# Optimization experiments

Measured on AMD Instinct MI355X. Metric: run time of the kernel, lower is better.

The kernel has to match this reference:

```python
import jax, jax.numpy as jnp
import numpy as np

B, T, D = 4, 4096, 2048
K = 1024
H, KVH, HD = 16, 4, 128
FF = 8192
EPS = 1e-6


def _rmsnorm(x, w):
    v = jnp.mean(x * x, axis=-1, keepdims=True)
    return x * jax.lax.rsqrt(v + EPS) * w


def _rotate_half(x):
    x1, x2 = jnp.split(x, 2, axis=-1)
    return jnp.concatenate([-x2, x1], axis=-1)


def setup_inputs() -> dict:
    key = jax.random.key(0)
    ks = jax.random.split(key, 16)
    hidden_states = jax.random.normal(ks[0], (B, T, D), dtype=jnp.float32)
    # unique sorted indices per sequence (top-k selection without duplicates)
    scores = jax.random.uniform(ks[1], (B, T))
    topk_indices = jnp.sort(jax.lax.top_k(scores, K)[1], axis=-1).astype(jnp.int64)
    gating_scores = jax.random.uniform(ks[2], (B, K), dtype=jnp.float32)
    # rotary embeddings over the full sequence [B, T, HD]
    inv = 1.0 / (10000.0 ** (jnp.arange(0, HD, 2, dtype=jnp.float32) / HD))
    ang = jnp.arange(T, dtype=jnp.float32)[:, None] * inv[None, :]  # [T, HD/2]
    emb = jnp.concatenate([ang, ang], axis=-1)
    cos = jnp.broadcast_to(jnp.cos(emb)[None], (B, T, HD)).astype(jnp.float32)
    sin = jnp.broadcast_to(jnp.sin(emb)[None], (B, T, HD)).astype(jnp.float32)
    s = 0.02
    params = dict(
        Wq=jax.random.normal(ks[3], (D, H * HD)) * s,
        bq=jnp.zeros((H * HD,)),
        Wk=jax.random.normal(ks[4], (D, KVH * HD)) * s,
        bk=jnp.zeros((KVH * HD,)),
        Wv=jax.random.normal(ks[5], (D, KVH * HD)) * s,
        bv=jnp.zeros((KVH * HD,)),
        Wo=jax.random.normal(ks[6], (H * HD, D)) * s,
        w_gate=jax.random.normal(ks[7], (D, FF)) * s,
        w_up=jax.random.normal(ks[8], (D, FF)) * s,
        w_down=jax.random.normal(ks[9], (FF, D)) * s,
        ln1_w=jnp.ones((D,)),
        ln2_w=jnp.ones((D,)),
    )
    return dict(hidden_states=hidden_states, topk_indices=topk_indices,
                gating_scores=gating_scores, cos=cos, sin=sin, **params)


def _decoder_layer(x, cos_s, sin_s, Wq, bq, Wk, bk, Wv, bv, Wo,
                   w_gate, w_up, w_down, ln1_w, ln2_w):
    # x: [B, K, D]; cos_s/sin_s: [B, K, HD]
    res = x
    h = _rmsnorm(x, ln1_w)
    q = (h @ Wq + bq).reshape(B, K, H, HD)
    k = (h @ Wk + bk).reshape(B, K, KVH, HD)
    v = (h @ Wv + bv).reshape(B, K, KVH, HD)
    c = cos_s[:, :, None, :]
    s = sin_s[:, :, None, :]
    q = q * c + _rotate_half(q) * s
    k = k * c + _rotate_half(k) * s
    # GQA: repeat kv heads
    k = jnp.repeat(k, H // KVH, axis=2)
    v = jnp.repeat(v, H // KVH, axis=2)
    scores = jnp.einsum('bqhd,bkhd->bhqk', q, k) / np.sqrt(HD)
    causal = jnp.tril(jnp.ones((K, K), dtype=bool))
    scores = jnp.where(causal[None, None], scores, jnp.finfo(scores.dtype).min)
    attn = jax.nn.softmax(scores, axis=-1)
    out = jnp.einsum('bhqk,bkhd->bqhd', attn, v).reshape(B, K, H * HD)
    x = res + out @ Wo
    # MLP (SwiGLU)
    res = x
    h = _rmsnorm(x, ln2_w)
    x = res + (jax.nn.silu(h @ w_gate) * (h @ w_up)) @ w_down
    return x


def reference(hidden_states, topk_indices, gating_scores, cos, sin,
              Wq, bq, Wk, bk, Wv, bv, Wo, w_gate, w_up, w_down, ln1_w, ln2_w):
    idx = topk_indices[:, :, None]  # [B, K, 1]
    selected = jnp.take_along_axis(hidden_states, idx, axis=1)  # [B, K, D]
    cos_s = jnp.take_along_axis(cos, idx, axis=1)
    sin_s = jnp.take_along_axis(sin, idx, axis=1)
    processed = _decoder_layer(selected, cos_s, sin_s, Wq, bq, Wk, bk, Wv, bv,
                               Wo, w_gate, w_up, w_down, ln1_w, ln2_w)
    # soft gating: selected + gate * (processed - selected)
    updated = selected + (processed - selected) * gating_scores[:, :, None]
    b_idx = jnp.arange(B)[:, None]
    final = hidden_states.at[b_idx, topk_indices].set(updated)
    return final
```

## Files before the change

kernel.cpp:

```cpp
#include <hip/hip_runtime.h>
#include <stdint.h>

typedef __bf16 bf16;
typedef __attribute__((ext_vector_type(8))) __bf16 bf16x8;
typedef __attribute__((ext_vector_type(4))) float f32x4;

namespace {

constexpr int cB = 4, cT = 4096, cD = 2048, cK = 1024, cH = 16, cKVH = 4, cHD = 128, cFF = 8192;
constexpr int cM = cB * cK;
constexpr int QKVW = cH * cHD + 2 * cKVH * cHD;

__device__ __forceinline__ void load_lds16(const void* g, void* l) {
  __builtin_amdgcn_global_load_lds((const __attribute__((address_space(1))) void*)g,
                                   (__attribute__((address_space(3))) void*)l, 16, 0, 0);
}

template <int N>
__device__ __forceinline__ void waitcnt_vm() {
  if constexpr (N == 0) asm volatile("s_waitcnt vmcnt(0)" ::: "memory");
  else if constexpr (N == 3) asm volatile("s_waitcnt vmcnt(3)" ::: "memory");
  else if constexpr (N == 4) asm volatile("s_waitcnt vmcnt(4)" ::: "memory");
  else if constexpr (N == 6) asm volatile("s_waitcnt vmcnt(6)" ::: "memory");
  else if constexpr (N == 8) asm volatile("s_waitcnt vmcnt(8)" ::: "memory");
  else if constexpr (N == 9) asm volatile("s_waitcnt vmcnt(9)" ::: "memory");
  else if constexpr (N == 12) asm volatile("s_waitcnt vmcnt(12)" ::: "memory");
  else static_assert(N == 0, "unsupported vmcnt literal");
}

template <int OP>
__device__ __forceinline__ float blk_reduce(float v) {
  __shared__ float sm[5];
  const int tid = threadIdx.x, lane = tid & 63, wid = tid >> 6;
#pragma unroll
  for (int o = 32; o; o >>= 1) {
    float o2 = __shfl_down(v, o, 64);
    v = OP ? fmaxf(v, o2) : v + o2;
  }
  if (lane == 0) sm[wid] = v;
  __syncthreads();
  if (tid == 0) {
    float r = sm[0];
#pragma unroll
    for (int i = 1; i < 4; ++i) r = OP ? fmaxf(r, sm[i]) : r + sm[i];
    sm[4] = r;
  }
  __syncthreads();
  float r = sm[4];
  __syncthreads();
  return r;
}

template <int BN, int WM, int WN, int RING, int UNROLL, class Epi>
__global__ __launch_bounds__(512, 2)
void gemm256(const bf16* __restrict__ A, int lda,
             const bf16* __restrict__ Bm, int ldb,
             int Kd, int GM, Epi epi) {
  constexpr int BM = 256;
  constexpr int FM = BM / WM / 16;
  constexpr int FN = BN / WN / 16;
  constexpr int ACALLS = 2;
  constexpr int BCALLS = BN / 128;
  constexpr int L = ACALLS + BCALLS;
  constexpr int D = RING - 1;
  constexpr int SLOTA = BM * 64;
  constexpr int SLOTB = BN * 64;
  constexpr int SLOT = SLOTA + SLOTB;
  __shared__ __align__(16) char lds[RING * SLOT];

  const int tid = threadIdx.x;
  const int lane = tid & 63;
  const int wid = tid >> 6;
  const int l15 = lane & 15, lq = lane >> 4;
  const int wr = wid / WN, wc = wid % WN;

  const int nwg = gridDim.x;
  const int xcd = blockIdx.x & 7, loc = blockIdx.x >> 3;
  const int wg = xcd * (nwg >> 3) + loc;
  const int GN = nwg / GM;
  const int per = 8 * GN;
  const int g = wg / per, r = wg % per;
  const int bm = g * 8 + (r & 7);
  const int bn = r >> 3;

  const bf16* Abase = A + (int64_t)bm * BM * lda;
  const bf16* Bbase = Bm + (int64_t)bn * BN * ldb;

  const bf16* srcA[ACALLS];
  int dstA[ACALLS];
#pragma unroll
  for (int c2 = 0; c2 < ACALLS; ++c2) {
    const int chunk = c2 * 512 + tid;
    const int row = chunk >> 2, pc = chunk & 3;
    const int lc = pc ^ ((row >> 1) & 3);
    srcA[c2] = Abase + (int64_t)row * lda + lc * 8;
    dstA[c2] = chunk * 16;
  }
  const bf16* srcB[BCALLS];
  int dstB[BCALLS];
#pragma unroll
  for (int c2 = 0; c2 < BCALLS; ++c2) {
    const int chunk = c2 * 512 + tid;
    const int row = chunk >> 2, pc = chunk & 3;
    const int lc = pc ^ ((row >> 1) & 3);
    srcB[c2] = Bbase + (int64_t)row * ldb + lc * 8;
    dstB[c2] = chunk * 16;
  }

  int offA[FM], offB[FN];
#pragma unroll
  for (int m = 0; m < FM; ++m) {
    const int row = wr * (BM / WM) + m * 16 + l15;
    offA[m] = row * 64 + (lq ^ ((row >> 1) & 3)) * 16;
  }
#pragma unroll
  for (int n = 0; n < FN; ++n) {
    const int row = wc * (BN / WN) + n * 16 + l15;
    offB[n] = SLOTA + row * 64 + (lq ^ ((row >> 1) & 3)) * 16;
  }

  const int KT = Kd >> 5;
  auto stage = [&](int t) {
    char* sb = lds + (size_t)(t % RING) * SLOT;
#pragma unroll
    for (int c2 = 0; c2 < ACALLS; ++c2)
      load_lds16(srcA[c2] + t * 32, sb + dstA[c2]);
#pragma unroll
    for (int c2 = 0; c2 < BCALLS; ++c2)
      load_lds16(srcB[c2] + t * 32, sb + SLOTA + dstB[c2]);
  };
  auto compute = [&](int t, f32x4 (&acc)[FM][FN]) {
    const char* sb = lds + (size_t)(t % RING) * SLOT;
    bf16x8 av[FM], bv[FN];
#pragma unroll
    for (int m = 0; m < FM; ++m) av[m] = *(const bf16x8*)(sb + offA[m]);
#pragma unroll
    for (int n = 0; n < FN; ++n) bv[n] = *(const bf16x8*)(sb + offB[n]);
    __builtin_amdgcn_s_setprio(1);
#pragma unroll
    for (int m = 0; m < FM; ++m)
#pragma unroll
      for (int n = 0; n < FN; ++n)
        acc[m][n] = __builtin_amdgcn_mfma_f32_16x16x32_bf16(av[m], bv[n], acc[m][n], 0, 0, 0);
    __builtin_amdgcn_s_setprio(0);
  };

  f32x4 acc[FM][FN] = {};

  if constexpr (UNROLL == 1) {
#pragma unroll
    for (int i = 0; i < D; ++i) stage(i);
    waitcnt_vm<(D - 1) * L>();
    __builtin_amdgcn_s_barrier();
    __builtin_amdgcn_sched_barrier(0);
    for (int t = 0; t < KT - D; ++t) {
      stage(t + D);
      compute(t, acc);
      waitcnt_vm<(D - 1) * L>();
      __builtin_amdgcn_s_barrier();
      __builtin_amdgcn_sched_barrier(0);
    }
    waitcnt_vm<0>();
    __builtin_amdgcn_s_barrier();
    for (int t = KT - D; t < KT; ++t) compute(t, acc);
  } else {
    static_assert(RING == 5 && UNROLL == 2, "pair mode is RING=5");
#pragma unroll
    for (int i = 0; i < 3; ++i) stage(i);
    waitcnt_vm<L>();
    __builtin_amdgcn_s_barrier();
    __builtin_amdgcn_sched_barrier(0);
    int t = 0;
    for (; t <= KT - 6; t += 2) {
      stage(t + 3);
      stage(t + 4);
      compute(t, acc);
      compute(t + 1, acc);
      waitcnt_vm<L>();
      __builtin_amdgcn_s_barrier();
      __builtin_amdgcn_sched_barrier(0);
    }
    stage(KT - 1);
    waitcnt_vm<0>();
    __builtin_amdgcn_s_barrier();
    compute(KT - 4, acc);
    compute(KT - 3, acc);
    compute(KT - 2, acc);
    compute(KT - 1, acc);
  }

#pragma unroll
  for (int m = 0; m < FM; ++m) {
    const int r0 = bm * BM + wr * (BM / WM) + m * 16 + lq * 4;
#pragma unroll
    for (int n = 0; n < FN; ++n) {
      const int c1 = bn * BN + wc * (BN / WN) + n * 16 + l15;
#pragma unroll
      for (int j = 0; j < 4; ++j) epi(r0 + j, c1, acc[m][n][j]);
    }
  }
}

__global__ __launch_bounds__(512, 2)
void gemm_gateup(const bf16* __restrict__ A, const bf16* __restrict__ Bg,
                 const bf16* __restrict__ Bu, bf16* __restrict__ act) {
  constexpr int BM = 256, BN = 128, WM = 4, WN = 2;
  constexpr int FM = 4, FN = 4;
  constexpr int RING = 4, D = 3, L = 4;
  constexpr int SLOTA = BM * 64, SLOTB = BN * 64;
  constexpr int SLOT = SLOTA + 2 * SLOTB;
  __shared__ __align__(16) char lds[RING * SLOT];

  const int tid = threadIdx.x;
  const int lane = tid & 63;
  const int wid = tid >> 6;
  const int l15 = lane & 15, lq = lane >> 4;
  const int wr = wid / WN, wc = wid % WN;

  const int nwg = gridDim.x;
  const int xcd = blockIdx.x & 7, loc = blockIdx.x >> 3;
  const int wg = xcd * (nwg >> 3) + loc;
  const int GM = 16, GN = nwg / GM;
  const int per = 8 * GN;
  const int g = wg / per, r = wg % per;
  const int bm = g * 8 + (r & 7);
  const int bn = r >> 3;

  const bf16* Abase = A + (int64_t)bm * BM * cD;
  const bf16* Gbase = Bg + (int64_t)bn * BN * cD;
  const bf16* Ubase = Bu + (int64_t)bn * BN * cD;

  const bf16* srcA[2];
  int dstA[2];
#pragma unroll
  for (int c2 = 0; c2 < 2; ++c2) {
    const int chunk = c2 * 512 + tid;
    const int row = chunk >> 2, pc = chunk & 3;
    const int lc = pc ^ ((row >> 1) & 3);
    srcA[c2] = Abase + (int64_t)row * cD + lc * 8;
    dstA[c2] = chunk * 16;
  }
  const int brow = tid >> 2, bpc = tid & 3;
  const int blc = bpc ^ ((brow >> 1) & 3);
  const bf16* srcG = Gbase + (int64_t)brow * cD + blc * 8;
  const bf16* srcU = Ubase + (int64_t)brow * cD + blc * 8;
  const int dstBo = tid * 16;

  int offA[FM], offB[FN];
#pragma unroll
  for (int m = 0; m < FM; ++m) {
    const int row = wr * 64 + m * 16 + l15;
    offA[m] = row * 64 + (lq ^ ((row >> 1) & 3)) * 16;
  }
#pragma unroll
  for (int n = 0; n < FN; ++n) {
    const int row = wc * 64 + n * 16 + l15;
    offB[n] = row * 64 + (lq ^ ((row >> 1) & 3)) * 16;
  }

  const int KT = cD >> 5;
  auto stage = [&](int t) {
    char* sb = lds + (size_t)(t % RING) * SLOT;
#pragma unroll
    for (int c2 = 0; c2 < 2; ++c2) load_lds16(srcA[c2] + t * 32, sb + dstA[c2]);
    load_lds16(srcG + t * 32, sb + SLOTA + dstBo);
    load_lds16(srcU + t * 32, sb + SLOTA + SLOTB + dstBo);
  };

  f32x4 accg[FM][FN] = {}, accu[FM][FN] = {};

  auto compute = [&](int t) {
    const char* sb = lds + (size_t)(t % RING) * SLOT;
    bf16x8 av[FM], gv[FN], uv[FN];
#pragma unroll
    for (int m = 0; m < FM; ++m) av[m] = *(const bf16x8*)(sb + offA[m]);
#pragma unroll
    for (int n = 0; n < FN; ++n) gv[n] = *(const bf16x8*)(sb + SLOTA + offB[n]);
#pragma unroll
    for (int n = 0; n < FN; ++n) uv[n] = *(const bf16x8*)(sb + SLOTA + SLOTB + offB[n]);
    __builtin_amdgcn_s_setprio(1);
#pragma unroll
    for (int m = 0; m < FM; ++m)
#pragma unroll
      for (int n = 0; n < FN; ++n) {
        accg[m][n] = __builtin_amdgcn_mfma_f32_16x16x32_bf16(av[m], gv[n], accg[m][n], 0, 0, 0);
        accu[m][n] = __builtin_amdgcn_mfma_f32_16x16x32_bf16(av[m], uv[n], accu[m][n], 0, 0, 0);
      }
    __builtin_amdgcn_s_setprio(0);
  };

#pragma unroll
  for (int i = 0; i < D; ++i) stage(i);
  waitcnt_vm<(D - 1) * L>();
  __builtin_amdgcn_s_barrier();
  __builtin_amdgcn_sched_barrier(0);
  for (int t = 0; t < KT - D; ++t) {
    stage(t + D);
    compute(t);
    waitcnt_vm<(D - 1) * L>();
    __builtin_amdgcn_s_barrier();
    __builtin_amdgcn_sched_barrier(0);
  }
  waitcnt_vm<0>();
  __builtin_amdgcn_s_barrier();
  for (int t = KT - D; t < KT; ++t) compute(t);

#pragma unroll
  for (int m = 0; m < FM; ++m) {
    const int r0 = bm * BM + wr * 64 + m * 16 + lq * 4;
#pragma unroll
    for (int n = 0; n < FN; ++n) {
      const int c1 = bn * BN + wc * 64 + n * 16 + l15;
#pragma unroll
      for (int j = 0; j < 4; ++j) {
        float gvv = accg[m][n][j];
        float s = gvv / (1.f + __expf(-gvv));
        act[(int64_t)(r0 + j) * cFF + c1] = (bf16)(s * accu[m][n][j]);
      }
    }
  }
}

struct EpiQKV {
  bf16* out; const float* bias;
  __device__ void operator()(int r, int c, float v) const {
    out[(int64_t)r * QKVW + c] = (bf16)(v + bias[c]);
  }
};
struct EpiOProj {
  float* x; const float* hidden; const int* topk;
  __device__ void operator()(int r, int c, float v) const {
    int b = r >> 10;
    int t = topk[r];
    x[(int64_t)r * cD + c] = v + hidden[((int64_t)b * cT + t) * cD + c];
  }
};
struct EpiDown {
  float* out; const float* x; const float* hidden; const int* topk; const float* gating;
  __device__ void operator()(int r, int c, float v) const {
    int b = r >> 10;
    int t = topk[r];
    float x2 = v + x[(int64_t)r * cD + c];
    int64_t ho = ((int64_t)b * cT + t) * cD + c;
    float sel = hidden[ho];
    out[ho] = sel + (x2 - sel) * gating[r];
  }
};

__global__ __launch_bounds__(256, 2) void flash_attn(const bf16* __restrict__ qkv,
                                                     const bf16* __restrict__ vt,
                                                     bf16* __restrict__ outb) {
  constexpr int QB = 64, KVB = 128;
  __shared__ __align__(16) char lds[81920];
  char* sK = lds;
  char* sP = lds + 32768;
  char* sV = lds + 49152;

  const int qt = blockIdx.x, h = blockIdx.y, b = blockIdx.z;
  const int kvh = h >> 2;
  const int qlo = qt * QB;
  const int tid = threadIdx.x, lane = tid & 63, wid = tid >> 6;
  const int l15 = lane & 15, lq = lane >> 4;
  const int wid16 = wid * 16;

  const bf16* qbase = qkv + (int64_t)(b * cK + qlo) * QKVW + h * cHD;
  const bf16* kbase = qkv + (int64_t)(b * cK) * QKVW + cH * cHD + kvh * cHD;
  const bf16* vtbase = vt + (int64_t)(b * cKVH + kvh) * cHD * cK;

#pragma unroll
  for (int c2 = 0; c2 < 4; ++c2) {
    int chunk = c2 * 256 + tid;
    int row = chunk >> 4, c16 = chunk & 15;
    load_lds16(qbase + (int64_t)row * QKVW + (c16 ^ (row & 15)) * 8, sK + chunk * 16);
  }
  __syncthreads();
  bf16x8 qf[4];
  {
    const int row = wid16 + l15;
#pragma unroll
    for (int kt = 0; kt < 4; ++kt)
      qf[kt] = *(const bf16x8*)(sK + row * 256 + (((kt * 4 + lq) ^ (row & 15)) * 16));
  }
  __syncthreads();

  f32x4 oacc[8] = {};
  float m_run[4], l_run[4];
#pragma unroll
  for (int j = 0; j < 4; ++j) { m_run[j] = -3.0e38f; l_run[j] = 0.f; }

  const int jmax = (qlo + QB - 1) >> 7;
  const float sl2e = 0.08838834764831845f * 1.44269504088896f;

  for (int jj = 0; jj <= jmax; ++jj) {
#pragma unroll
    for (int c2 = 0; c2 < 8; ++c2) {
      int chunk = c2 * 256 + tid;
      int row = chunk >> 4, c16 = chunk & 15;
      int cs = (c16 ^ (row & 15)) * 8;
      load_lds16(kbase + (int64_t)(jj * KVB + row) * QKVW + cs, sK + chunk * 16);
      load_lds16(vtbase + (int64_t)row * cK + jj * KVB + cs, sV + chunk * 16);
    }
    __syncthreads();

    f32x4 sacc[8] = {};
#pragma unroll
    for (int kt = 0; kt < 4; ++kt) {
      bf16x8 bv[8];
#pragma unroll
      for (int n = 0; n < 8; ++n) {
        int rk = n * 16 + l15;
        bv[n] = *(const bf16x8*)(sK + rk * 256 + (((kt * 4 + lq) ^ (rk & 15)) * 16));
      }
#pragma unroll
      for (int n = 0; n < 8; ++n)
        sacc[n] = __builtin_amdgcn_mfma_f32_16x16x32_bf16(qf[kt], bv[n], sacc[n], 0, 0, 0);
    }

    if (jj == jmax) {
#pragma unroll
      for (int n = 0; n < 8; ++n)
#pragma unroll
        for (int j = 0; j < 4; ++j) {
          int qrow = qlo + wid16 + lq * 4 + j;
          int kcol = jj * KVB + n * 16 + l15;
          if (kcol > qrow) sacc[n][j] = -3.0e38f;
        }
    }

#pragma unroll
    for (int j = 0; j < 4; ++j) {
      float mx = sacc[0][j];
#pragma unroll
      for (int n = 1; n < 8; ++n) mx = fmaxf(mx, sacc[n][j]);
#pragma unroll
      for (int off = 1; off < 16; off <<= 1) mx = fmaxf(mx, __shfl_xor(mx, off, 64));
      float mnew = fmaxf(m_run[j], mx);
      float corr = exp2f((m_run[j] - mnew) * sl2e);
      m_run[j] = mnew;
      float ps = 0.f;
#pragma unroll
      for (int n = 0; n < 8; ++n) {
        float p = exp2f((sacc[n][j] - mnew) * sl2e);
        sacc[n][j] = p;
        ps += p;
      }
#pragma unroll
      for (int off = 1; off < 16; off <<= 1) ps += __shfl_xor(ps, off, 64);
      l_run[j] = l_run[j] * corr + ps;
#pragma unroll
      for (int n = 0; n < 8; ++n) oacc[n][j] *= corr;
    }

#pragma unroll
    for (int n = 0; n < 8; ++n)
#pragma unroll
      for (int j = 0; j < 4; ++j) {
        int row = wid16 + lq * 4 + j;
        int col = n * 16 + l15;
        int c16 = (col >> 3) ^ (row & 15);
        *(bf16*)(sP + row * 256 + c16 * 16 + (col & 7) * 2) = (bf16)sacc[n][j];
      }
    __syncthreads();

#pragma unroll
    for (int kt = 0; kt < 4; ++kt) {
      const int prow = wid16 + l15;
      bf16x8 av = *(const bf16x8*)(sP + prow * 256 + (((kt * 4 + lq) ^ (prow & 15)) * 16));
      bf16x8 bv[8];
#pragma unroll
      for (int n = 0; n < 8; ++n) {
        int rd = n * 16 + l15;
        bv[n] = *(const bf16x8*)(sV + rd * 256 + (((kt * 4 + lq) ^ (rd & 15)) * 16));
      }
#pragma unroll
      for (int n = 0; n < 8; ++n)
        oacc[n] = __builtin_amdgcn_mfma_f32_16x16x32_bf16(av, bv[n], oacc[n], 0, 0, 0);
    }
    __syncthreads();
  }

#pragma unroll
  for (int j = 0; j < 4; ++j) {
    int row = qlo + wid16 + lq * 4 + j;
    float inv = 1.f / l_run[j];
#pragma unroll
    for (int n = 0; n < 8; ++n) {
      int col = h * cHD + n * 16 + l15;
      outb[((int64_t)b * cK + row) * cD + col] = (bf16)(oacc[n][j] * inv);
    }
  }
}

__global__ void copy_f4(const float4* __restrict__ s, float4* __restrict__ d, int64_t n) {
  int64_t i = (int64_t)blockIdx.x * blockDim.x + threadIdx.x;
  const int64_t st = (int64_t)gridDim.x * blockDim.x;
  for (; i < n; i += st) d[i] = s[i];
}

__global__ void wconv(const float* __restrict__ src, bf16* __restrict__ dst,
                      int R, int C, int coff, int ldd) {
  __shared__ float t[32][33];
  const int c0 = blockIdx.x * 32, r0 = blockIdx.y * 32;
  for (int rr = threadIdx.y; rr < 32; rr += 8)
    t[rr][threadIdx.x] = src[(int64_t)(r0 + rr) * C + c0 + threadIdx.x];
  __syncthreads();
  for (int rr = threadIdx.y; rr < 32; rr += 8)
    dst[(int64_t)(c0 + rr + coff) * ldd + r0 + threadIdx.x] = (bf16)t[threadIdx.x][rr];
}

__global__ void biascat(const float* __restrict__ bq, const float* __restrict__ bk,
                        const float* __restrict__ bv, float* __restrict__ o) {
  int i = blockIdx.x * 256 + threadIdx.x;
  if (i < QKVW) o[i] = (i < 2048) ? bq[i] : (i < 2560 ? bk[i - 2048] : bv[i - 2560]);
}

__global__ void rmsnorm_rows(const float* __restrict__ base, const int* __restrict__ topk,
                             const float* __restrict__ w, bf16* __restrict__ out) {
  const int r = blockIdx.x;
  const float* src;
  if (topk) {
    int t = topk[r];
    src = base + ((int64_t)(r >> 10) * cT + t) * cD;
  } else {
    src = base + (int64_t)r * cD;
  }
  const int tid = threadIdx.x;
  const float4* s4 = (const float4*)src;
  float4 a = s4[tid * 2], b = s4[tid * 2 + 1];
  float ss = a.x * a.x + a.y * a.y + a.z * a.z + a.w * a.w +
             b.x * b.x + b.y * b.y + b.z * b.z + b.w * b.w;
  float tot = blk_reduce<0>(ss);
  float sc = rsqrtf(tot * (1.f / cD) + 1e-6f);
  bf16* o = out + (int64_t)r * cD;
  const int d0 = tid * 8;
  o[d0 + 0] = (bf16)(a.x * sc * w[d0 + 0]);
  o[d0 + 1] = (bf16)(a.y * sc * w[d0 + 1]);
  o[d0 + 2] = (bf16)(a.z * sc * w[d0 + 2]);
  o[d0 + 3] = (bf16)(a.w * sc * w[d0 + 3]);
  o[d0 + 4] = (bf16)(b.x * sc * w[d0 + 4]);
  o[d0 + 5] = (bf16)(b.y * sc * w[d0 + 5]);
  o[d0 + 6] = (bf16)(b.z * sc * w[d0 + 6]);
  o[d0 + 7] = (bf16)(b.w * sc * w[d0 + 7]);
}

__global__ void rope_kernel(bf16* __restrict__ qkv, const float* __restrict__ cosb,
                            const float* __restrict__ sinb, const int* __restrict__ topk) {
  const int r = blockIdx.x;
  const int b = r >> 10;
  const int t = topk[r];
  const float* cr = cosb + ((int64_t)b * cT + t) * cHD;
  const float* sr = sinb + ((int64_t)b * cT + t) * cHD;
  bf16* rowq = qkv + (int64_t)r * QKVW;
  for (int p = threadIdx.x; p < (cH + cKVH) * 64; p += 256) {
    int hh = p >> 6, d = p & 63;
    bf16* base = (hh < cH) ? (rowq + hh * cHD) : (rowq + cH * cHD + (hh - cH) * cHD);
    float x1 = (float)base[d], x2 = (float)base[d + 64];
    float c1 = cr[d], s1 = sr[d], c2 = cr[d + 64], s2 = sr[d + 64];
    base[d] = (bf16)(x1 * c1 - x2 * s1);
    base[d + 64] = (bf16)(x2 * c2 + x1 * s2);
  }
}

__global__ void vtrans(const bf16* __restrict__ qkv, bf16* __restrict__ Vt) {
  __shared__ bf16 t[32][33];
  const int bz = blockIdx.z, b = bz >> 2, kv = bz & 3;
  const int k0 = blockIdx.x * 32, d0 = blockIdx.y * 32;
  for (int rr = threadIdx.y; rr < 32; rr += 8)
    t[rr][threadIdx.x] =
        qkv[(int64_t)(b * cK + k0 + rr) * QKVW + cH * cHD + cKVH * cHD + kv * cHD + d0 + threadIdx.x];
  __syncthreads();
  for (int rr = threadIdx.y; rr < 32; rr += 8)
    Vt[((int64_t)(b * cKVH + kv) * cHD + d0 + rr) * cK + k0 + threadIdx.x] = t[threadIdx.x][rr];
}

}

extern "C" void kernel_launch(void* const* d_in, const int* in_sizes, int n_in,
                              void* d_out, int out_size, void* d_ws, size_t ws_size,
                              hipStream_t stream) {
  const float* hidden = (const float*)d_in[0];
  const int* topk = (const int*)d_in[1];
  const float* gating = (const float*)d_in[2];
  const float* cosb = (const float*)d_in[3];
  const float* sinb = (const float*)d_in[4];
  const float* Wq = (const float*)d_in[5];
  const float* bq = (const float*)d_in[6];
  const float* Wk = (const float*)d_in[7];
  const float* bk = (const float*)d_in[8];
  const float* Wv = (const float*)d_in[9];
  const float* bv = (const float*)d_in[10];
  const float* Wo = (const float*)d_in[11];
  const float* wg = (const float*)d_in[12];
  const float* wu = (const float*)d_in[13];
  const float* wd = (const float*)d_in[14];
  const float* ln1 = (const float*)d_in[15];
  const float* ln2 = (const float*)d_in[16];
  float* out = (float*)d_out;
  (void)in_sizes; (void)n_in; (void)out_size; (void)ws_size;

  char* ws = (char*)d_ws;
  size_t off = 0;
  auto alloc = [&](size_t bytes) {
    char* p = ws + off;
    off += (bytes + 255) & ~(size_t)255;
    return p;
  };
  bf16* wt_qkv = (bf16*)alloc((size_t)QKVW * cD * 2);
  bf16* wt_o = (bf16*)alloc((size_t)cD * cD * 2);
  bf16* wt_g = (bf16*)alloc((size_t)cFF * cD * 2);
  bf16* wt_u = (bf16*)alloc((size_t)cFF * cD * 2);
  bf16* wt_d = (bf16*)alloc((size_t)cD * cFF * 2);
  float* bias_cat = (float*)alloc((size_t)QKVW * 4);
  bf16* hbuf = (bf16*)alloc((size_t)cM * cD * 2);
  bf16* qkv = (bf16*)alloc((size_t)cM * QKVW * 2);
  bf16* vt = (bf16*)alloc((size_t)cB * cKVH * cHD * cK * 2);
  bf16* attnout = (bf16*)alloc((size_t)cM * cD * 2);
  float* xbuf = (float*)alloc((size_t)cM * cD * 4);
  bf16* actbuf = (bf16*)alloc((size_t)cM * cFF * 2);

  copy_f4<<<2048, 256, 0, stream>>>((const float4*)hidden, (float4*)out,
                                    (int64_t)cB * cT * cD / 4);

  const dim3 tb(32, 8);
  wconv<<<dim3(cD / 32, cD / 32), tb, 0, stream>>>(Wq, wt_qkv, cD, cD, 0, cD);
  wconv<<<dim3(512 / 32, cD / 32), tb, 0, stream>>>(Wk, wt_qkv, cD, 512, 2048, cD);
  wconv<<<dim3(512 / 32, cD / 32), tb, 0, stream>>>(Wv, wt_qkv, cD, 512, 2560, cD);
  wconv<<<dim3(cD / 32, cD / 32), tb, 0, stream>>>(Wo, wt_o, cD, cD, 0, cD);
  wconv<<<dim3(cFF / 32, cD / 32), tb, 0, stream>>>(wg, wt_g, cD, cFF, 0, cD);
  wconv<<<dim3(cFF / 32, cD / 32), tb, 0, stream>>>(wu, wt_u, cD, cFF, 0, cD);
  wconv<<<dim3(cD / 32, cFF / 32), tb, 0, stream>>>(wd, wt_d, cFF, cD, 0, cFF);
  biascat<<<(QKVW + 255) / 256, 256, 0, stream>>>(bq, bk, bv, bias_cat);

  rmsnorm_rows<<<cM, 256, 0, stream>>>(hidden, topk, ln1, hbuf);
  gemm256<256, 2, 4, 4, 1, EpiQKV><<<16 * (QKVW / 256), 512, 0, stream>>>(
      hbuf, cD, wt_qkv, cD, cD, 16, EpiQKV{qkv, bias_cat});
  rope_kernel<<<cM, 256, 0, stream>>>(qkv, cosb, sinb, topk);
  vtrans<<<dim3(cK / 32, cHD / 32, cB * cKVH), tb, 0, stream>>>(qkv, vt);

  flash_attn<<<dim3(cK / 64, cH, cB), 256, 0, stream>>>(qkv, vt, attnout);

  gemm256<128, 4, 2, 5, 2, EpiOProj><<<16 * (cD / 128), 512, 0, stream>>>(
      attnout, cD, wt_o, cD, cD, 16, EpiOProj{xbuf, hidden, topk});
  rmsnorm_rows<<<cM, 256, 0, stream>>>(xbuf, nullptr, ln2, hbuf);
  gemm_gateup<<<16 * (cFF / 128), 512, 0, stream>>>(hbuf, wt_g, wt_u, actbuf);
  gemm256<128, 4, 2, 5, 2, EpiDown><<<16 * (cD / 128), 512, 0, stream>>>(
      actbuf, cFF, wt_d, cFF, cFF, 16, EpiDown{out, xbuf, hidden, topk, gating});
}
```

Baseline: 868.2 us.

## Deepen gate/up GEMM pipeline, skip copying selected rows, retune QKV GEMM

The gate/up GEMM gets a 5-slot LDS ring and its main loop now issues two stages and runs two compute steps per barrier, halving the number of barriers. A new flags kernel marks the top-k rows so the initial hidden-to-output copy skips rows that the down-projection epilogue overwrites anyway, cutting memory traffic. The QKV GEMM template parameters change to a deeper ring and different pipeline depth. In exchange, the larger ring uses more LDS, and the memset plus flags kernel add two small launches.

```diff
diff --git a/kernel.cpp b/kernel.cpp
--- a/kernel.cpp
+++ b/kernel.cpp
@@ -206,7 +206,7 @@
                  const bf16* __restrict__ Bu, bf16* __restrict__ act) {
   constexpr int BM = 256, BN = 128, WM = 4, WN = 2;
   constexpr int FM = 4, FN = 4;
-  constexpr int RING = 4, D = 3, L = 4;
+  constexpr int RING = 5, L = 4;
   constexpr int SLOTA = BM * 64, SLOTB = BN * 64;
   constexpr int SLOT = SLOTA + 2 * SLOTB;
   __shared__ __align__(16) char lds[RING * SLOT];
@@ -290,20 +290,27 @@
   };
 
 #pragma unroll
-  for (int i = 0; i < D; ++i) stage(i);
-  waitcnt_vm<(D - 1) * L>();
+  for (int i = 0; i < 3; ++i) stage(i);
+  waitcnt_vm<L>();
   __builtin_amdgcn_s_barrier();
   __builtin_amdgcn_sched_barrier(0);
-  for (int t = 0; t < KT - D; ++t) {
-    stage(t + D);
+  int t = 0;
+  for (; t <= KT - 6; t += 2) {
+    stage(t + 3);
+    stage(t + 4);
     compute(t);
-    waitcnt_vm<(D - 1) * L>();
+    compute(t + 1);
+    waitcnt_vm<L>();
     __builtin_amdgcn_s_barrier();
     __builtin_amdgcn_sched_barrier(0);
   }
+  stage(KT - 1);
   waitcnt_vm<0>();
   __builtin_amdgcn_s_barrier();
-  for (int t = KT - D; t < KT; ++t) compute(t);
+  compute(KT - 4);
+  compute(KT - 3);
+  compute(KT - 2);
+  compute(KT - 1);
 
 #pragma unroll
   for (int m = 0; m < FM; ++m) {
@@ -491,10 +498,19 @@
   }
 }
 
-__global__ void copy_f4(const float4* __restrict__ s, float4* __restrict__ d, int64_t n) {
+__global__ void copy_skip(const float4* __restrict__ s, float4* __restrict__ d,
+                          const unsigned char* __restrict__ flags, int64_t n) {
   int64_t i = (int64_t)blockIdx.x * blockDim.x + threadIdx.x;
   const int64_t st = (int64_t)gridDim.x * blockDim.x;
-  for (; i < n; i += st) d[i] = s[i];
+  for (; i < n; i += st) {
+    int row = (int)(i >> 9);
+    if (!flags[row]) d[i] = s[i];
+  }
+}
+
+__global__ void build_flags(const int* __restrict__ topk, unsigned char* __restrict__ flags) {
+  int r = blockIdx.x * 256 + threadIdx.x;
+  if (r < cM) flags[(r >> 10) * cT + topk[r]] = 1;
 }
 
 __global__ void wconv(const float* __restrict__ src, bf16* __restrict__ dst,
@@ -617,9 +633,12 @@
   bf16* attnout = (bf16*)alloc((size_t)cM * cD * 2);
   float* xbuf = (float*)alloc((size_t)cM * cD * 4);
   bf16* actbuf = (bf16*)alloc((size_t)cM * cFF * 2);
-
-  copy_f4<<<2048, 256, 0, stream>>>((const float4*)hidden, (float4*)out,
-                                    (int64_t)cB * cT * cD / 4);
+  unsigned char* flags = (unsigned char*)alloc((size_t)cB * cT);
+
+  hipMemsetAsync(flags, 0, (size_t)cB * cT, stream);
+  build_flags<<<cM / 256, 256, 0, stream>>>(topk, flags);
+  copy_skip<<<2048, 256, 0, stream>>>((const float4*)hidden, (float4*)out, flags,
+                                      (int64_t)cB * cT * cD / 4);
 
   const dim3 tb(32, 8);
   wconv<<<dim3(cD / 32, cD / 32), tb, 0, stream>>>(Wq, wt_qkv, cD, cD, 0, cD);
@@ -632,7 +651,7 @@
   biascat<<<(QKVW + 255) / 256, 256, 0, stream>>>(bq, bk, bv, bias_cat);
 
   rmsnorm_rows<<<cM, 256, 0, stream>>>(hidden, topk, ln1, hbuf);
-  gemm256<256, 2, 4, 4, 1, EpiQKV><<<16 * (QKVW / 256), 512, 0, stream>>>(
+  gemm256<256, 2, 4, 5, 2, EpiQKV><<<16 * (QKVW / 256), 512, 0, stream>>>(
       hbuf, cD, wt_qkv, cD, cD, 16, EpiQKV{qkv, bias_cat});
   rope_kernel<<<cM, 256, 0, stream>>>(qkv, cosb, sinb, topk);
   vtrans<<<dim3(cK / 32, cHD / 32, cB * cKVH), tb, 0, stream>>>(qkv, vt);
```

Result: no change. 869.5 us (+0.2%).
